# Performance work log

Measured on AMD Instinct MI355X. Metric: run time of the kernel, lower is better.

The kernel has to match this reference:

```python
import jax, jax.numpy as jnp
from jax import lax
import numpy as np

WINDOW = 51
HALF = WINDOW // 2  # 25
K_SAUVOLA = 0.2     # skimage threshold_sauvola default k
RGB_W = np.array([0.2989, 0.5870, 0.1140], dtype=np.float32)  # tf.image.rgb_to_grayscale weights


def _window_sum(x, axis):
    """Sliding-window sum of length WINDOW along `axis`, 'same' size, reflect padding.
    O(1) per pixel via cumulative sums (integral-image style), matching the
    uniform_filter-based local statistics in skimage's Sauvola."""
    pad = [(0, 0)] * x.ndim
    pad[axis] = (HALF, HALF)
    xp = jnp.pad(x, pad, mode='reflect')
    cs = jnp.cumsum(xp, axis=axis)
    zshape = list(cs.shape)
    zshape[axis] = 1
    cs = jnp.concatenate([jnp.zeros(zshape, cs.dtype), cs], axis=axis)
    n = cs.shape[axis]
    hi = lax.slice_in_dim(cs, WINDOW, n, axis=axis)
    lo = lax.slice_in_dim(cs, 0, n - WINDOW, axis=axis)
    return hi - lo


def _box_mean(x):
    # separable 51x51 box filter over H (axis 1) and W (axis 2)
    s = _window_sum(_window_sum(x, axis=1), axis=2)
    return s / jnp.asarray(WINDOW * WINDOW, x.dtype)


def setup_inputs() -> dict:
    key = jax.random.key(0)
    inputs = jax.random.uniform(key, (8, 1024, 1024, 3), dtype=jnp.float32)
    return {"inputs": inputs}


def reference(inputs) -> jnp.ndarray:
    # RGB -> grayscale (channels == 3 branch), keep channel dim [B,H,W,1]
    gray = jnp.einsum('bhwc,c->bhw', inputs, jnp.asarray(RGB_W))[..., None]
    # local mean / std over 51x51 window
    m = _box_mean(gray)
    m2 = _box_mean(gray * gray)
    var = jnp.maximum(m2 - m * m, 0.0)
    s = jnp.sqrt(var)
    # skimage default dynamic range: r = 0.5 * (max - min) over the whole array
    r = 0.5 * (jnp.max(gray) - jnp.min(gray))
    thresh = m * (1.0 + K_SAUVOLA * (s / r - 1.0))
    # (gray > thresh) * 1
    return (gray > thresh).astype(jnp.float32)
```

## Files before the change

### kernel.cpp

```cpp
#include <hip/hip_runtime.h>

#define IMW 1024
#define IMH 1024
#define NB  8
#define HALF 25
#define STRIP 32
#define NCELL 64

#define W_R ((double)0.2989f)
#define W_G ((double)0.5870f)
#define W_B ((double)0.1140f)
#define INV_AREA (1.0 / 2601.0)

__device__ __forceinline__ int refl(int i, int n) {
    if (i < 0) i = -i;
    if (i >= n) i = 2 * n - 2 - i;
    return i;
}

__device__ __forceinline__ int pidx(int i) { return i + 2 * (i >> 3); }

__device__ __forceinline__ double wsum(const double* __restrict__ C, int p) {
    int a = p + HALF; if (a > IMW - 1) a = IMW - 1;
    int b = p - HALF - 1;
    double s = C[pidx(a)] - (b >= 0 ? C[pidx(b)] : 0.0);
    if (p <= HALF - 1)      s += C[pidx(HALF - p)] - C[pidx(0)];
    if (p >= IMW - HALF)    s += C[pidx(IMW - 2)] - C[pidx(2*IMW - 2 - HALF - 1 - p)];
    return s;
}

__global__ void k0_init(unsigned* cells) {
    cells[threadIdx.x] = (threadIdx.x < NCELL) ? 0xFFFFFFFFu : 0u;
}

__global__ __launch_bounds__(256) void k1_rowpass(const float* __restrict__ in,
                                                  float2* __restrict__ hp,
                                                  float* __restrict__ gray,
                                                  unsigned* __restrict__ cells) {
    __shared__ double cs1[1280];
    __shared__ double cs2[1280];
    __shared__ double wt1[4], wt2[4];
    __shared__ float bmin[4], bmax[4];
    const int row = blockIdx.x;
    const long long base = (long long)row * IMW;
    const int t = threadIdx.x;
    const int lane = t & 63, w = t >> 6;

    const float4* p4 = (const float4*)(in + base * 3);
    float4 f0 = p4[3*t], f1 = p4[3*t+1], f2 = p4[3*t+2];
    double g0 = (double)f0.x*W_R + (double)f0.y*W_G + (double)f0.z*W_B;
    double g1 = (double)f0.w*W_R + (double)f1.x*W_G + (double)f1.y*W_B;
    double g2 = (double)f1.z*W_R + (double)f1.w*W_G + (double)f2.x*W_B;
    double g3 = (double)f2.y*W_R + (double)f2.z*W_G + (double)f2.w*W_B;
    float gf0 = (float)g0, gf1 = (float)g1, gf2 = (float)g2, gf3 = (float)g3;

    ((float4*)(gray + base))[t] = make_float4(gf0, gf1, gf2, gf3);

    double l1_0 = g0, l1_1 = l1_0 + g1, l1_2 = l1_1 + g2, l1_3 = l1_2 + g3;
    double l2_0 = g0*g0, l2_1 = l2_0 + g1*g1, l2_2 = l2_1 + g2*g2, l2_3 = l2_2 + g3*g3;

    float lmin = fminf(fminf(gf0, gf1), fminf(gf2, gf3));
    float lmax = fmaxf(fmaxf(gf0, gf1), fmaxf(gf2, gf3));
    for (int off = 32; off; off >>= 1) {
        lmin = fminf(lmin, __shfl_down(lmin, off));
        lmax = fmaxf(lmax, __shfl_down(lmax, off));
    }
    if (lane == 0) { bmin[w] = lmin; bmax[w] = lmax; }

    double v1 = l1_3, v2 = l2_3;
    for (int off = 1; off < 64; off <<= 1) {
        double u1 = __shfl_up(v1, off);
        double u2 = __shfl_up(v2, off);
        if (lane >= off) { v1 += u1; v2 += u2; }
    }
    if (lane == 63) { wt1[w] = v1; wt2[w] = v2; }
    __syncthreads();
    double e1 = v1 - l1_3, e2 = v2 - l2_3;
    for (int j = 0; j < w; j++) { e1 += wt1[j]; e2 += wt2[j]; }

    const int ci = 4 * t + 2 * (t >> 1);
    double2* c1 = (double2*)&cs1[ci];
    double2* c2 = (double2*)&cs2[ci];
    c1[0] = make_double2(e1 + l1_0, e1 + l1_1);
    c1[1] = make_double2(e1 + l1_2, e1 + l1_3);
    c2[0] = make_double2(e2 + l2_0, e2 + l2_1);
    c2[1] = make_double2(e2 + l2_2, e2 + l2_3);

    if (t == 0) {
        float m0 = fminf(fminf(bmin[0], bmin[1]), fminf(bmin[2], bmin[3]));
        float m1 = fmaxf(fmaxf(bmax[0], bmax[1]), fmaxf(bmax[2], bmax[3]));
        int cell = row & (NCELL - 1);
        atomicMin(&cells[cell], __float_as_uint(m0));
        atomicMax(&cells[NCELL + cell], __float_as_uint(m1));
    }
    __syncthreads();

    for (int k = 0; k < 4; k++) {
        int p = t + 256 * k;
        hp[base + p] = make_float2((float)wsum(cs1, p), (float)wsum(cs2, p));
    }
}

__global__ __launch_bounds__(256) void k2_colpass(const float* __restrict__ gray,
                                                  const float2* __restrict__ hp,
                                                  const unsigned* __restrict__ cells,
                                                  float* __restrict__ out) {
    __shared__ double sr[2];
    const int t = threadIdx.x;
    if (t < 64) {
        unsigned mn = cells[t];
        unsigned mx = cells[NCELL + t];
        for (int off = 32; off; off >>= 1) {
            unsigned a = __shfl_down(mn, off);
            unsigned b = __shfl_down(mx, off);
            mn = (a < mn) ? a : mn;
            mx = (b > mx) ? b : mx;
        }
        if (t == 0) {
            sr[0] = (double)__uint_as_float(mn);
            sr[1] = (double)__uint_as_float(mx);
        }
    }
    __syncthreads();
    const double r  = 0.5 * (sr[1] - sr[0]);
    const double r2 = r * r;

    const int id   = blockIdx.x;
    const int b    = id & 7;
    const int rest = id >> 3;
    const int ys   = rest & 31;
    const int xc   = rest >> 5;
    const int x  = xc * 256 + t;
    const int y0 = ys * STRIP;
    const long long ib = (long long)b * IMH * IMW;

    double vx = 0.0, vy = 0.0;

    if (ys >= 1 && ys <= 30) {
        const float2* ph = hp + ib + (long long)(y0 - HALF) * IMW + x;
        #pragma unroll 17
        for (int j = 0; j < 51; j++) {
            float2 h = ph[0];
            vx += (double)h.x; vy += (double)h.y;
            ph += IMW;
        }
        const float2* pa = hp + ib + (long long)(y0 + HALF + 1) * IMW + x;
        const float2* ps = hp + ib + (long long)(y0 - HALF) * IMW + x;
        const float*  pg = gray + ib + (long long)y0 * IMW + x;
        float*        po = out  + ib + (long long)y0 * IMW + x;
        #pragma unroll 8
        for (int i = 0; i < STRIP; i++) {
            float2 ha = pa[0];
            float2 hs = ps[0];
            double g = (double)pg[0];

            double m  = vx * INV_AREA;
            double va = fmax(vy * INV_AREA - m * m, 0.0);
            double A  = g - 0.8 * m;
            int o = (A > 0.0) && (A * A * r2 > 0.04 * m * m * va);
            po[0] = o ? 1.0f : 0.0f;

            vx += (double)ha.x - (double)hs.x;
            vy += (double)ha.y - (double)hs.y;
            pa += IMW; ps += IMW; pg += IMW; po += IMW;
        }
    } else {
        #pragma unroll 8
        for (int j = -HALF; j <= HALF; j++) {
            int ry = refl(y0 + j, IMH);
            float2 h = hp[ib + (long long)ry * IMW + x];
            vx += (double)h.x; vy += (double)h.y;
        }
        #pragma unroll 8
        for (int y = y0; y < y0 + STRIP; y++) {
            long long pix = ib + (long long)y * IMW + x;
            double g = (double)gray[pix];

            double m  = vx * INV_AREA;
            double va = fmax(vy * INV_AREA - m * m, 0.0);
            double A  = g - 0.8 * m;
            int o = (A > 0.0) && (A * A * r2 > 0.04 * m * m * va);
            out[pix] = o ? 1.0f : 0.0f;

            int ra = refl(y + HALF + 1, IMH);
            int rs = refl(y - HALF, IMH);
            float2 ha = hp[ib + (long long)ra * IMW + x];
            float2 hs = hp[ib + (long long)rs * IMW + x];
            vx += (double)ha.x - (double)hs.x;
            vy += (double)ha.y - (double)hs.y;
        }
    }
}

extern "C" void kernel_launch(void* const* d_in, const int* in_sizes, int n_in,
                              void* d_out, int out_size, void* d_ws, size_t ws_size,
                              hipStream_t stream) {
    const float* in = (const float*)d_in[0];
    float* out = (float*)d_out;

    unsigned* cells = (unsigned*)d_ws;
    float2* hp = (float2*)((char*)d_ws + 4096);
    float* gray = (float*)((char*)d_ws + 4096
                           + (size_t)NB * IMH * IMW * sizeof(float2));

    hipLaunchKernelGGL(k0_init, dim3(1), dim3(2 * NCELL), 0, stream, cells);
    hipLaunchKernelGGL(k1_rowpass, dim3(NB * IMH), dim3(256), 0, stream,
                       in, hp, gray, cells);
    hipLaunchKernelGGL(k2_colpass, dim3((IMW / 256) * (IMH / STRIP) * NB), dim3(256), 0, stream,
                       gray, hp, cells, out);
}
```

Baseline: 208.7 us.

## Process each row with a single wavefront holding 16 pixels per thread

The row-pass kernel now uses one 64-thread wavefront per image row instead of four. Each thread handles 16 consecutive pixels, so the prefix sum needs only one wave-level scan and the cross-wave shared-memory combine and one barrier go away. Prefix sums go into shared memory in a transposed layout to avoid bank conflicts, and the horizontal sums are written as contiguous float4 stores. In exchange, register pressure per thread rises and each block has fewer threads to hide memory latency. The input loads also become strided across threads, which may hurt coalescing.

```diff
diff --git a/kernel.cpp b/kernel.cpp
--- a/kernel.cpp
+++ b/kernel.cpp
@@ -18,14 +18,14 @@
     return i;
 }
 
-__device__ __forceinline__ int pidx(int i) { return i + 2 * (i >> 3); }
-
-__device__ __forceinline__ double wsum(const double* __restrict__ C, int p) {
+__device__ __forceinline__ int tphys(int a) { return (a & 15) * 64 + (a >> 4); }
+
+__device__ __forceinline__ double twsum(const double* __restrict__ T, int p) {
     int a = p + HALF; if (a > IMW - 1) a = IMW - 1;
     int b = p - HALF - 1;
-    double s = C[pidx(a)] - (b >= 0 ? C[pidx(b)] : 0.0);
-    if (p <= HALF - 1)      s += C[pidx(HALF - p)] - C[pidx(0)];
-    if (p >= IMW - HALF)    s += C[pidx(IMW - 2)] - C[pidx(2*IMW - 2 - HALF - 1 - p)];
+    double s = T[tphys(a)] - (b >= 0 ? T[tphys(b)] : 0.0);
+    if (p <= HALF - 1)      s += T[tphys(HALF - p)] - T[tphys(0)];
+    if (p >= IMW - HALF)    s += T[tphys(IMW - 2)] - T[tphys(2*IMW - 2 - HALF - 1 - p)];
     return s;
 }
 
@@ -33,72 +33,81 @@
     cells[threadIdx.x] = (threadIdx.x < NCELL) ? 0xFFFFFFFFu : 0u;
 }
 
-__global__ __launch_bounds__(256) void k1_rowpass(const float* __restrict__ in,
-                                                  float2* __restrict__ hp,
-                                                  float* __restrict__ gray,
-                                                  unsigned* __restrict__ cells) {
-    __shared__ double cs1[1280];
-    __shared__ double cs2[1280];
-    __shared__ double wt1[4], wt2[4];
-    __shared__ float bmin[4], bmax[4];
+__global__ __launch_bounds__(64) void k1_rowpass(const float* __restrict__ in,
+                                                 float2* __restrict__ hp,
+                                                 float* __restrict__ gray,
+                                                 unsigned* __restrict__ cells) {
+    __shared__ double T1[IMW];
+    __shared__ double T2[IMW];
+    const int t = threadIdx.x;
     const int row = blockIdx.x;
     const long long base = (long long)row * IMW;
-    const int t = threadIdx.x;
-    const int lane = t & 63, w = t >> 6;
+    const int p0 = 16 * t;
 
     const float4* p4 = (const float4*)(in + base * 3);
-    float4 f0 = p4[3*t], f1 = p4[3*t+1], f2 = p4[3*t+2];
-    double g0 = (double)f0.x*W_R + (double)f0.y*W_G + (double)f0.z*W_B;
-    double g1 = (double)f0.w*W_R + (double)f1.x*W_G + (double)f1.y*W_B;
-    double g2 = (double)f1.z*W_R + (double)f1.w*W_G + (double)f2.x*W_B;
-    double g3 = (double)f2.y*W_R + (double)f2.z*W_G + (double)f2.w*W_B;
-    float gf0 = (float)g0, gf1 = (float)g1, gf2 = (float)g2, gf3 = (float)g3;
-
-    ((float4*)(gray + base))[t] = make_float4(gf0, gf1, gf2, gf3);
-
-    double l1_0 = g0, l1_1 = l1_0 + g1, l1_2 = l1_1 + g2, l1_3 = l1_2 + g3;
-    double l2_0 = g0*g0, l2_1 = l2_0 + g1*g1, l2_2 = l2_1 + g2*g2, l2_3 = l2_2 + g3*g3;
-
-    float lmin = fminf(fminf(gf0, gf1), fminf(gf2, gf3));
-    float lmax = fmaxf(fmaxf(gf0, gf1), fmaxf(gf2, gf3));
+    float g[16];
+    #pragma unroll
+    for (int k = 0; k < 4; k++) {
+        float4 a = p4[12*t + 3*k + 0];
+        float4 b = p4[12*t + 3*k + 1];
+        float4 c = p4[12*t + 3*k + 2];
+        g[4*k+0] = (float)((double)a.x*W_R + (double)a.y*W_G + (double)a.z*W_B);
+        g[4*k+1] = (float)((double)a.w*W_R + (double)b.x*W_G + (double)b.y*W_B);
+        g[4*k+2] = (float)((double)b.z*W_R + (double)b.w*W_G + (double)c.x*W_B);
+        g[4*k+3] = (float)((double)c.y*W_R + (double)c.z*W_G + (double)c.w*W_B);
+    }
+    #pragma unroll
+    for (int k = 0; k < 4; k++)
+        ((float4*)(gray + base))[4*t + k] =
+            make_float4(g[4*k+0], g[4*k+1], g[4*k+2], g[4*k+3]);
+
+    float lmin = g[0], lmax = g[0];
+    #pragma unroll
+    for (int j = 1; j < 16; j++) { lmin = fminf(lmin, g[j]); lmax = fmaxf(lmax, g[j]); }
     for (int off = 32; off; off >>= 1) {
         lmin = fminf(lmin, __shfl_down(lmin, off));
         lmax = fmaxf(lmax, __shfl_down(lmax, off));
     }
-    if (lane == 0) { bmin[w] = lmin; bmax[w] = lmax; }
-
-    double v1 = l1_3, v2 = l2_3;
+    if (t == 0) {
+        int cell = row & (NCELL - 1);
+        atomicMin(&cells[cell], __float_as_uint(lmin));
+        atomicMax(&cells[NCELL + cell], __float_as_uint(lmax));
+    }
+
+    double C1[16], C2[16];
+    double v1 = 0.0, v2 = 0.0;
+    #pragma unroll
+    for (int j = 0; j < 16; j++) {
+        double d = (double)g[j];
+        v1 += d; v2 = fma(d, d, v2);
+        C1[j] = v1; C2[j] = v2;
+    }
+
+    double s1 = v1, s2 = v2;
     for (int off = 1; off < 64; off <<= 1) {
-        double u1 = __shfl_up(v1, off);
-        double u2 = __shfl_up(v2, off);
-        if (lane >= off) { v1 += u1; v2 += u2; }
-    }
-    if (lane == 63) { wt1[w] = v1; wt2[w] = v2; }
+        double u1 = __shfl_up(s1, off);
+        double u2 = __shfl_up(s2, off);
+        if (t >= off) { s1 += u1; s2 += u2; }
+    }
+    double e1 = s1 - v1, e2 = s2 - v2;
+
+    #pragma unroll
+    for (int j = 0; j < 16; j++) {
+        T1[j * 64 + t] = e1 + C1[j];
+        T2[j * 64 + t] = e2 + C2[j];
+    }
     __syncthreads();
-    double e1 = v1 - l1_3, e2 = v2 - l2_3;
-    for (int j = 0; j < w; j++) { e1 += wt1[j]; e2 += wt2[j]; }
-
-    const int ci = 4 * t + 2 * (t >> 1);
-    double2* c1 = (double2*)&cs1[ci];
-    double2* c2 = (double2*)&cs2[ci];
-    c1[0] = make_double2(e1 + l1_0, e1 + l1_1);
-    c1[1] = make_double2(e1 + l1_2, e1 + l1_3);
-    c2[0] = make_double2(e2 + l2_0, e2 + l2_1);
-    c2[1] = make_double2(e2 + l2_2, e2 + l2_3);
-
-    if (t == 0) {
-        float m0 = fminf(fminf(bmin[0], bmin[1]), fminf(bmin[2], bmin[3]));
-        float m1 = fmaxf(fmaxf(bmax[0], bmax[1]), fmaxf(bmax[2], bmax[3]));
-        int cell = row & (NCELL - 1);
-        atomicMin(&cells[cell], __float_as_uint(m0));
-        atomicMax(&cells[NCELL + cell], __float_as_uint(m1));
-    }
-    __syncthreads();
-
-    for (int k = 0; k < 4; k++) {
-        int p = t + 256 * k;
-        hp[base + p] = make_float2((float)wsum(cs1, p), (float)wsum(cs2, p));
-    }
+
+    float hx[16], hy[16];
+    #pragma unroll
+    for (int j = 0; j < 16; j++) {
+        hx[j] = (float)twsum(T1, p0 + j);
+        hy[j] = (float)twsum(T2, p0 + j);
+    }
+    float4* o = (float4*)(hp + base + p0);
+    #pragma unroll
+    for (int k = 0; k < 8; k++)
+        o[k] = make_float4(hx[2*k], hy[2*k], hx[2*k+1], hy[2*k+1]);
 }
 
 __global__ __launch_bounds__(256) void k2_colpass(const float* __restrict__ gray,
@@ -204,7 +213,7 @@
                            + (size_t)NB * IMH * IMW * sizeof(float2));
 
     hipLaunchKernelGGL(k0_init, dim3(1), dim3(2 * NCELL), 0, stream, cells);
-    hipLaunchKernelGGL(k1_rowpass, dim3(NB * IMH), dim3(256), 0, stream,
+    hipLaunchKernelGGL(k1_rowpass, dim3(NB * IMH), dim3(64), 0, stream,
                        in, hp, gray, cells);
     hipLaunchKernelGGL(k2_colpass, dim3((IMW / 256) * (IMH / STRIP) * NB), dim3(256), 0, stream,
                        gray, hp, cells, out);
```

Result: slower. 221.8 us (+6.3%).
